# Kernel tuning notes

Measured on AMD Instinct MI355X. Metric: run time of the kernel, lower is better.

## Reference

```python
import jax, jax.numpy as jnp
import numpy as np

B, CM, CT, CA, H, W = 4, 256, 64, 128, 80, 80


def setup_inputs() -> dict:
    key = jax.random.key(0)
    ks = jax.random.split(key, 10)
    s = lambda fan_in: 1.0 / np.sqrt(fan_in)
    return {
        "met_features": jax.random.normal(ks[0], (B, CM, H, W), jnp.float32),
        "terrain_features": jax.random.normal(ks[1], (B, CT, H, W), jnp.float32),
        "wq": jax.random.normal(ks[2], (CA, CM), jnp.float32) * s(CM),
        "bq": jax.random.normal(ks[3], (CA,), jnp.float32) * s(CM),
        "wk": jax.random.normal(ks[4], (CA, CT), jnp.float32) * s(CT),
        "bk": jax.random.normal(ks[5], (CA,), jnp.float32) * s(CT),
        "wv": jax.random.normal(ks[6], (CA, CT), jnp.float32) * s(CT),
        "bv": jax.random.normal(ks[7], (CA,), jnp.float32) * s(CT),
        "wo": jax.random.normal(ks[8], (CM, CA), jnp.float32) * s(CA),
        "bo": jax.random.normal(ks[9], (CM,), jnp.float32) * s(CA),
    }


def reference(met_features, terrain_features, wq, bq, wk, bk, wv, bv, wo, bo):
    b, c, h, w = met_features.shape
    n = h * w  # tokens
    scale = CA ** (-0.5)
    # 1x1 convs == per-pixel linear: [B,Cin,N] -> [B,Cattn,N]
    met = met_features.reshape(b, c, n)
    ter = terrain_features.reshape(b, terrain_features.shape[1], n)
    q = jnp.einsum('oc,bcn->bon', wq, met) + bq[None, :, None]
    k = jnp.einsum('oc,bcn->bon', wk, ter) + bk[None, :, None]
    v = jnp.einsum('oc,bcn->bon', wv, ter) + bv[None, :, None]
    # attn[b, i, j] = sum_c q[b,c,i] * k[b,c,j]
    attn = jax.nn.softmax(jnp.einsum('bci,bcj->bij', q, k) * scale, axis=-1)
    # out[b, c, i] = sum_j v[b,c,j] * attn[b,i,j]
    out = jnp.einsum('bcj,bij->bci', v, attn)
    out = jnp.einsum('oc,bcn->bon', wo, out) + bo[None, :, None]
    return met_features + out.reshape(b, c, h, w)
```

## Files before the change

kernel.cpp:

```cpp
#include <hip/hip_runtime.h>
#include <hip/hip_bf16.h>

#define BB 4
#define CMv 256
#define CTv 64
#define CAv 128
#define NTOK 6400
#define KVSPLIT 5
#define KVRANGE 1280
#define NTILES 20
#define QSCL 0.12753102198064644f

typedef unsigned short u16;
typedef __attribute__((ext_vector_type(8))) short sh8;
typedef __attribute__((ext_vector_type(4))) float f32x4;
typedef __attribute__((ext_vector_type(16))) float f32x16;
typedef __attribute__((ext_vector_type(4))) unsigned uint4v;
typedef __attribute__((ext_vector_type(2))) unsigned uint2v;

__device__ __forceinline__ u16 f2bf(float f) {
  return __builtin_bit_cast(u16, __float2bfloat16(f));
}
__device__ __forceinline__ float bf2f(u16 x) {
  unsigned u = ((unsigned)x) << 16;
  return __builtin_bit_cast(float, u);
}
__device__ __forceinline__ unsigned pk2(float a, float b) {
  unsigned r;
  asm("v_cvt_pk_bf16_f32 %0, %1, %2" : "=v"(r) : "v"(a), "v"(b));
  return r;
}
__device__ __forceinline__ f32x16 zero16() {
  f32x16 z;
#pragma unroll
  for (int i = 0; i < 16; i++) z[i] = 0.f;
  return z;
}
typedef const __attribute__((address_space(1))) unsigned int* gas_p;
typedef __attribute__((address_space(3))) unsigned int* las_p;
__device__ __forceinline__ void gl_lds16(const u16* g, u16* l) {
  __builtin_amdgcn_global_load_lds((gas_p)g, (las_p)l, 16, 0, 0);
}

__global__ __launch_bounds__(256) void prep(const float* __restrict__ wq,
                                            const float* __restrict__ bq,
                                            const float* __restrict__ wk,
                                            const float* __restrict__ wv,
                                            const float* __restrict__ wo,
                                            u16* __restrict__ wqB,
                                            float* __restrict__ bqs,
                                            u16* __restrict__ wkB,
                                            u16* __restrict__ wvB,
                                            u16* __restrict__ woB) {
  const int i0 = blockIdx.x * 256 + threadIdx.x;
  const int stride = gridDim.x * 256;
  for (int i = i0; i < 128 * 256; i += stride) wqB[i] = f2bf(wq[i] * QSCL);
  for (int i = i0; i < 128 * 64; i += stride) { wkB[i] = f2bf(wk[i]); wvB[i] = f2bf(wv[i]); }
  for (int i = i0; i < 256 * 128; i += stride) woB[i] = f2bf(wo[i]);
  for (int i = i0; i < 128; i += stride) bqs[i] = bq[i] * QSCL;
}

__global__ __launch_bounds__(512, 2) void qkvproj(const float* __restrict__ met,
                                                  const float* __restrict__ ter,
                                                  const u16* __restrict__ wqB,
                                                  const float* __restrict__ bqs,
                                                  const u16* __restrict__ wkB,
                                                  const float* __restrict__ bk,
                                                  const u16* __restrict__ wvB,
                                                  const float* __restrict__ bv,
                                                  u16* __restrict__ Qtm,
                                                  u16* __restrict__ Ktm,
                                                  u16* __restrict__ Vcm) {
  const int tid = threadIdx.x;
  const int w = tid >> 6;
  const int lane = tid & 63;
  const int l31 = lane & 31;
  const int h = lane >> 5;

  if (blockIdx.x < 200) {
    const int b = blockIdx.x / 50;
    const int tokb = (blockIdx.x % 50) * 128;
    const int chg = (w & 3) * 32;
    const int half = w >> 2;
    const u16* wb = wqB + (size_t)(chg + l31) * 256 + h * 8;
    sh8 af[16];
#pragma unroll
    for (int kk = 0; kk < 16; kk++) af[kk] = *(const sh8*)(wb + kk * 16);
    float bias[16];
#pragma unroll
    for (int r = 0; r < 16; r++) bias[r] = bqs[chg + (r & 3) + 8 * (r >> 2) + 4 * h];
    const float* mp = met + (size_t)b * CMv * NTOK;
#pragma unroll
    for (int ct = 0; ct < 2; ct++) {
      const int tok = tokb + (half * 2 + ct) * 32 + l31;
      f32x16 acc = zero16();
#pragma unroll
      for (int kk = 0; kk < 16; kk++) {
        const float* cp = mp + (size_t)(kk * 16 + 8 * h) * NTOK + tok;
        float x0 = cp[0], x1 = cp[(size_t)NTOK], x2 = cp[(size_t)2 * NTOK],
              x3 = cp[(size_t)3 * NTOK], x4 = cp[(size_t)4 * NTOK],
              x5 = cp[(size_t)5 * NTOK], x6 = cp[(size_t)6 * NTOK],
              x7 = cp[(size_t)7 * NTOK];
        uint4v u = {pk2(x0, x1), pk2(x2, x3), pk2(x4, x5), pk2(x6, x7)};
        acc = __builtin_amdgcn_mfma_f32_32x32x16_bf16(
            af[kk], __builtin_bit_cast(sh8, u), acc, 0, 0, 0);
      }
      u16* qp = Qtm + ((size_t)b * NTOK + tok) * CAv;
#pragma unroll
      for (int rq = 0; rq < 4; rq++) {
        const int ch0 = chg + 8 * rq + 4 * h;
        uint2v d = {pk2(acc[4 * rq + 0] + bias[4 * rq + 0],
                        acc[4 * rq + 1] + bias[4 * rq + 1]),
                    pk2(acc[4 * rq + 2] + bias[4 * rq + 2],
                        acc[4 * rq + 3] + bias[4 * rq + 3])};
        *(uint2v*)(qp + ch0) = d;
      }
    }
  } else {
    const int bx = blockIdx.x - 200;
    const int b = bx / 50;
    const int tokb = (bx % 50) * 128;
    const bool isV = w >= 4;
    const int chg = (w & 3) * 32;
    const u16* wb = (isV ? wvB : wkB) + (size_t)(chg + l31) * 64 + h * 8;
    sh8 af[4];
#pragma unroll
    for (int kk = 0; kk < 4; kk++) af[kk] = *(const sh8*)(wb + kk * 16);
    const float* barr = isV ? bv : bk;
    float bias[16];
#pragma unroll
    for (int r = 0; r < 16; r++) bias[r] = barr[chg + (r & 3) + 8 * (r >> 2) + 4 * h];
    const float* tp = ter + (size_t)b * CTv * NTOK;
#pragma unroll
    for (int ct = 0; ct < 4; ct++) {
      const int tok = tokb + ct * 32 + l31;
      f32x16 acc = zero16();
#pragma unroll
      for (int kk = 0; kk < 4; kk++) {
        const float* cp = tp + (size_t)(kk * 16 + 8 * h) * NTOK + tok;
        float x0 = cp[0], x1 = cp[(size_t)NTOK], x2 = cp[(size_t)2 * NTOK],
              x3 = cp[(size_t)3 * NTOK], x4 = cp[(size_t)4 * NTOK],
              x5 = cp[(size_t)5 * NTOK], x6 = cp[(size_t)6 * NTOK],
              x7 = cp[(size_t)7 * NTOK];
        uint4v u = {pk2(x0, x1), pk2(x2, x3), pk2(x4, x5), pk2(x6, x7)};
        acc = __builtin_amdgcn_mfma_f32_32x32x16_bf16(
            af[kk], __builtin_bit_cast(sh8, u), acc, 0, 0, 0);
      }
      if (!isV) {
        u16* kp = Ktm + ((size_t)b * NTOK + tok) * CAv;
#pragma unroll
        for (int rq = 0; rq < 4; rq++) {
          const int ch0 = chg + 8 * rq + 4 * h;
          uint2v d = {pk2(acc[4 * rq + 0] + bias[4 * rq + 0],
                          acc[4 * rq + 1] + bias[4 * rq + 1]),
                      pk2(acc[4 * rq + 2] + bias[4 * rq + 2],
                          acc[4 * rq + 3] + bias[4 * rq + 3])};
          *(uint2v*)(kp + ch0) = d;
        }
      } else {
#pragma unroll
        for (int r = 0; r < 16; r++) {
          const int ch = chg + (r & 3) + 8 * (r >> 2) + 4 * h;
          Vcm[((size_t)b * CAv + ch) * NTOK + tok] = f2bf(acc[r] + bias[r]);
        }
      }
    }
  }
}

__global__ __launch_bounds__(512, 2) void attn(const u16* __restrict__ Qtm,
                                               const u16* __restrict__ Ktm,
                                               const u16* __restrict__ Vcm,
                                               u16* __restrict__ Opart,
                                               float* __restrict__ Lpart) {
  __shared__ __align__(16) unsigned char smem[65536];

  const int tid = threadIdx.x;
  const int w = tid >> 6;
  const int lane = tid & 63;
  const int l31 = lane & 31;
  const int h = lane >> 5;

  const int x = blockIdx.x & 7;
  const int W = x * 62 + (x < 4 ? x : 4) + (blockIdx.x >> 3);
  const int g = W / 25;
  const int qt = W % 25;
  const int b = g / KVSPLIT;
  const int kvq = g % KVSPLIT;
  const int qb0 = qt * 256;
  const int kv00 = kvq * KVRANGE;

  const u16* Qb = Qtm + ((size_t)b * NTOK + qb0 + w * 32 + l31) * CAv;
  const u16* Kb = Ktm + (size_t)b * NTOK * CAv;
  const u16* Vb = Vcm + (size_t)b * CAv * NTOK;

  sh8 qf[8];
#pragma unroll
  for (int kk = 0; kk < 8; kk++) qf[kk] = *(const sh8*)(Qb + kk * 16 + h * 8);

  const int kr0 = w * 8 + (lane >> 4);
  const int kr1 = kr0 + 4;
  const u16* ksrc0 = Kb + ((size_t)kv00 + kr0) * CAv + (((lane & 15) ^ (kr0 & 15)) * 8);
  const u16* ksrc1 = Kb + ((size_t)kv00 + kr1) * CAv + (((lane & 15) ^ (kr1 & 15)) * 8);
  const int vc = w * 16 + (lane >> 3);
  const u16* vsrc = Vb + (size_t)vc * NTOK + kv00 +
                    (((lane & 7) ^ ((lane >> 3) & 7)) * 8);

  int koff[8];
#pragma unroll
  for (int kk = 0; kk < 8; kk++)
    koff[kk] = l31 * 256 + (((2 * kk + h) ^ (l31 & 15)) << 4);
  int voff[4];
#pragma unroll
  for (int b2 = 0; b2 < 4; b2++)
    voff[b2] = l31 * 128 + (((2 * b2 + h) ^ (l31 & 7)) << 4);

#define STAGE(p)                                               \
  do {                                                         \
    u16* kb_ = (u16*)(smem + (p) * 32768) + w * 1024;          \
    gl_lds16(ksrc0, kb_);                                      \
    gl_lds16(ksrc1, kb_ + 512);                                \
    u16* vb_ = (u16*)(smem + (p) * 32768 + 16384) + w * 1024;  \
    gl_lds16(vsrc, vb_);                                       \
    gl_lds16(vsrc + (size_t)8 * NTOK, vb_ + 512);              \
    ksrc0 += 64 * CAv;                                         \
    ksrc1 += 64 * CAv;                                         \
    vsrc += 64;                                                \
  } while (0)

  STAGE(0);
  asm volatile("s_waitcnt vmcnt(0)" ::: "memory");
  __builtin_amdgcn_s_barrier();

  f32x16 o[4];
#pragma unroll
  for (int i = 0; i < 4; i++) o[i] = zero16();
  float lsum = 0.f;

  int buf = 0;
  for (int t = 0; t < NTILES; t++) {
    if (t < NTILES - 1) STAGE(buf ^ 1);
    const unsigned char* kbuf = smem + buf * 32768;
    const unsigned char* vbuf = kbuf + 16384;
    __builtin_amdgcn_s_setprio(1);
    f32x16 s0 = zero16(), s1 = zero16();
#pragma unroll
    for (int kk = 0; kk < 8; kk++) {
      sh8 kfa = *(const sh8*)(kbuf + koff[kk]);
      sh8 kfb = *(const sh8*)(kbuf + 8192 + koff[kk]);
      s0 = __builtin_amdgcn_mfma_f32_32x32x16_bf16(kfa, qf[kk], s0, 0, 0, 0);
      s1 = __builtin_amdgcn_mfma_f32_32x32x16_bf16(kfb, qf[kk], s1, 0, 0, 0);
    }
    __builtin_amdgcn_s_setprio(0);
    f32x16 p0, p1;
#pragma unroll
    for (int r = 0; r < 16; r++) {
      p0[r] = __builtin_exp2f(s0[r]);
      p1[r] = __builtin_exp2f(s1[r]);
    }
#pragma unroll
    for (int r = 0; r < 16; r++) lsum += p0[r] + p1[r];
    unsigned pkm0[4][2], pkm1[4][2];
#pragma unroll
    for (int rq = 0; rq < 4; rq++) {
      pkm0[rq][0] = pk2(p0[4 * rq + 0], p0[4 * rq + 1]);
      pkm0[rq][1] = pk2(p0[4 * rq + 2], p0[4 * rq + 3]);
      pkm1[rq][0] = pk2(p1[4 * rq + 0], p1[4 * rq + 1]);
      pkm1[rq][1] = pk2(p1[4 * rq + 2], p1[4 * rq + 3]);
    }
#pragma unroll
    for (int xx = 0; xx < 2; xx++) {
#pragma unroll
      for (int b2i = 0; b2i < 2; b2i++) {
        unsigned ow0, ow1, sd0, sd1;
        if (xx == 0) {
          ow0 = h ? pkm0[2 * b2i + 1][0] : pkm0[2 * b2i][0];
          ow1 = h ? pkm0[2 * b2i + 1][1] : pkm0[2 * b2i][1];
          sd0 = h ? pkm0[2 * b2i][0] : pkm0[2 * b2i + 1][0];
          sd1 = h ? pkm0[2 * b2i][1] : pkm0[2 * b2i + 1][1];
        } else {
          ow0 = h ? pkm1[2 * b2i + 1][0] : pkm1[2 * b2i][0];
          ow1 = h ? pkm1[2 * b2i + 1][1] : pkm1[2 * b2i][1];
          sd0 = h ? pkm1[2 * b2i][0] : pkm1[2 * b2i + 1][0];
          sd1 = h ? pkm1[2 * b2i][1] : pkm1[2 * b2i + 1][1];
        }
        unsigned rv0 = (unsigned)__shfl_xor((int)sd0, 32);
        unsigned rv1 = (unsigned)__shfl_xor((int)sd1, 32);
        uint4v fw = {h ? rv0 : ow0, h ? rv1 : ow1, h ? ow0 : rv0, h ? ow1 : rv1};
        sh8 pf = __builtin_bit_cast(sh8, fw);
        const int b2 = xx * 2 + b2i;
        __builtin_amdgcn_s_setprio(1);
#pragma unroll
        for (int ct = 0; ct < 4; ct++) {
          sh8 vf = *(const sh8*)(vbuf + ct * 4096 + voff[b2]);
          o[ct] = __builtin_amdgcn_mfma_f32_32x32x16_bf16(vf, pf, o[ct], 0, 0, 0);
        }
        __builtin_amdgcn_s_setprio(0);
      }
    }
    asm volatile("s_waitcnt vmcnt(0)" ::: "memory");
    __builtin_amdgcn_s_barrier();
    buf ^= 1;
  }
#undef STAGE

  lsum += __shfl_xor(lsum, 32);
  u16* op = Opart + (((size_t)kvq * BB + b) * NTOK + qb0 + w * 32 + l31) * CAv;
#pragma unroll
  for (int ct = 0; ct < 4; ct++)
#pragma unroll
    for (int rq = 0; rq < 4; rq++) {
      uint2v d = {pk2(o[ct][4 * rq + 0], o[ct][4 * rq + 1]),
                  pk2(o[ct][4 * rq + 2], o[ct][4 * rq + 3])};
      *(uint2v*)(op + ct * 32 + rq * 8 + h * 4) = d;
    }
  if (h == 0) {
    size_t mi = ((size_t)kvq * BB + b) * NTOK + qb0 + w * 32 + l31;
    Lpart[mi] = lsum;
  }
}

__global__ __launch_bounds__(512, 2) void outproj(const float* __restrict__ met,
                                                  const u16* __restrict__ woB,
                                                  const float* __restrict__ bo,
                                                  const u16* __restrict__ Opart,
                                                  const float* __restrict__ Lpart,
                                                  float* __restrict__ out) {
  const int tid = threadIdx.x;
  const int w = tid >> 6;
  const int lane = tid & 63;
  const int l31 = lane & 31;
  const int h = lane >> 5;

  const int b = blockIdx.x / 100;
  const int tokb = (blockIdx.x % 100) * 64;
  const int chg = (w & 3) * 64;
  const int ct = w >> 2;
  const int tok = tokb + ct * 32 + l31;
  const size_t n = (size_t)b * NTOK + tok;
  const size_t PSTR = (size_t)BB * NTOK;

  const u16* wb0 = woB + (size_t)(chg + l31) * 128 + h * 8;
  const u16* wb1 = woB + (size_t)(chg + 32 + l31) * 128 + h * 8;
  sh8 a0[8], a1[8];
#pragma unroll
  for (int kk = 0; kk < 8; kk++) {
    a0[kk] = *(const sh8*)(wb0 + kk * 16);
    a1[kk] = *(const sh8*)(wb1 + kk * 16);
  }

  float L = 0.f;
#pragma unroll
  for (int i = 0; i < KVSPLIT; i++) L += Lpart[i * PSTR + n];
  const float rL = 1.f / L;

  f32x16 acc0 = zero16(), acc1 = zero16();
#pragma unroll
  for (int kk = 0; kk < 8; kk++) {
    float s[8];
#pragma unroll
    for (int j = 0; j < 8; j++) s[j] = 0.f;
#pragma unroll
    for (int i = 0; i < KVSPLIT; i++) {
      sh8 v = *(const sh8*)(Opart + (i * PSTR + n) * CAv + kk * 16 + 8 * h);
#pragma unroll
      for (int j = 0; j < 8; j++) s[j] += bf2f((u16)v[j]);
    }
    uint4v u = {pk2(s[0] * rL, s[1] * rL), pk2(s[2] * rL, s[3] * rL),
                pk2(s[4] * rL, s[5] * rL), pk2(s[6] * rL, s[7] * rL)};
    sh8 bf = __builtin_bit_cast(sh8, u);
    acc0 = __builtin_amdgcn_mfma_f32_32x32x16_bf16(a0[kk], bf, acc0, 0, 0, 0);
    acc1 = __builtin_amdgcn_mfma_f32_32x32x16_bf16(a1[kk], bf, acc1, 0, 0, 0);
  }
#pragma unroll
  for (int r = 0; r < 16; r++) {
    const int ro = (r & 3) + 8 * (r >> 2) + 4 * h;
    const int ch0 = chg + ro;
    const int ch1 = chg + 32 + ro;
    size_t i0 = ((size_t)b * CMv + ch0) * NTOK + tok;
    size_t i1 = ((size_t)b * CMv + ch1) * NTOK + tok;
    out[i0] = met[i0] + acc0[r] + bo[ch0];
    out[i1] = met[i1] + acc1[r] + bo[ch1];
  }
}

extern "C" void kernel_launch(void* const* d_in, const int* in_sizes, int n_in,
                              void* d_out, int out_size, void* d_ws, size_t ws_size,
                              hipStream_t stream) {
  const float* met = (const float*)d_in[0];
  const float* ter = (const float*)d_in[1];
  const float* wq = (const float*)d_in[2];
  const float* bq = (const float*)d_in[3];
  const float* wk = (const float*)d_in[4];
  const float* bk = (const float*)d_in[5];
  const float* wv = (const float*)d_in[6];
  const float* bv = (const float*)d_in[7];
  const float* wo = (const float*)d_in[8];
  const float* bo = (const float*)d_in[9];
  float* out = (float*)d_out;

  u16* Qtm = (u16*)d_ws;
  u16* Ktm = Qtm + (size_t)BB * NTOK * CAv;
  u16* Vcm = Ktm + (size_t)BB * NTOK * CAv;
  u16* Opart = Vcm + (size_t)BB * NTOK * CAv;
  float* Lpart = (float*)(Opart + (size_t)KVSPLIT * BB * NTOK * CAv);
  u16* wqB = (u16*)(Lpart + (size_t)KVSPLIT * BB * NTOK);
  u16* wkB = wqB + 128 * 256;
  u16* wvB = wkB + 128 * 64;
  u16* woB = wvB + 128 * 64;
  float* bqs = (float*)(woB + 256 * 128);

  prep<<<dim3(40), dim3(256), 0, stream>>>(wq, bq, wk, wv, wo, wqB, bqs, wkB, wvB, woB);
  qkvproj<<<dim3(400), dim3(512), 0, stream>>>(met, ter, wqB, bqs, wkB, bk,
                                               wvB, bv, Qtm, Ktm, Vcm);
  attn<<<dim3(500), dim3(512), 0, stream>>>(Qtm, Ktm, Vcm, Opart, Lpart);
  outproj<<<dim3(400), dim3(512), 0, stream>>>(met, woB, bo, Opart, Lpart, out);
}
```

Baseline: 171.4 us.

## Triple-buffer smaller 32-key KV tiles to raise attention kernel occupancy

Halves the KV tile size from 64 to 32 keys per iteration, so each tile buffer uses 16KB. It switches from double to triple buffering with two tiles in flight, and partial vmcnt waits let loads overlap more. Total LDS drops to 48KB and launch bounds rise to 4 blocks per SM. In exchange there are twice as many barriers per KV range, less MFMA work between syncs, and more register pressure from the tighter launch bound.

```diff
diff --git a/kernel.cpp b/kernel.cpp
--- a/kernel.cpp
+++ b/kernel.cpp
@@ -8,7 +8,7 @@
 #define NTOK 6400
 #define KVSPLIT 5
 #define KVRANGE 1280
-#define NTILES 20
+#define NTILES 40
 #define QSCL 0.12753102198064644f
 
 typedef unsigned short u16;
@@ -168,12 +168,12 @@
   }
 }
 
-__global__ __launch_bounds__(512, 2) void attn(const u16* __restrict__ Qtm,
+__global__ __launch_bounds__(512, 4) void attn(const u16* __restrict__ Qtm,
                                                const u16* __restrict__ Ktm,
                                                const u16* __restrict__ Vcm,
                                                u16* __restrict__ Opart,
                                                float* __restrict__ Lpart) {
-  __shared__ __align__(16) unsigned char smem[65536];
+  __shared__ __align__(16) unsigned char smem[49152];
 
   const int tid = threadIdx.x;
   const int w = tid >> 6;
@@ -198,38 +198,34 @@
 #pragma unroll
   for (int kk = 0; kk < 8; kk++) qf[kk] = *(const sh8*)(Qb + kk * 16 + h * 8);
 
-  const int kr0 = w * 8 + (lane >> 4);
-  const int kr1 = kr0 + 4;
-  const u16* ksrc0 = Kb + ((size_t)kv00 + kr0) * CAv + (((lane & 15) ^ (kr0 & 15)) * 8);
-  const u16* ksrc1 = Kb + ((size_t)kv00 + kr1) * CAv + (((lane & 15) ^ (kr1 & 15)) * 8);
-  const int vc = w * 16 + (lane >> 3);
+  const int kr = w * 4 + (lane >> 4);
+  const u16* ksrc = Kb + ((size_t)kv00 + kr) * CAv + (((lane & 15) ^ (kr & 15)) * 8);
+  const int vc = w * 16 + (lane >> 2);
   const u16* vsrc = Vb + (size_t)vc * NTOK + kv00 +
-                    (((lane & 7) ^ ((lane >> 3) & 7)) * 8);
+                    (((lane & 3) ^ ((lane >> 3) & 3)) * 8);
 
   int koff[8];
 #pragma unroll
   for (int kk = 0; kk < 8; kk++)
     koff[kk] = l31 * 256 + (((2 * kk + h) ^ (l31 & 15)) << 4);
-  int voff[4];
-#pragma unroll
-  for (int b2 = 0; b2 < 4; b2++)
-    voff[b2] = l31 * 128 + (((2 * b2 + h) ^ (l31 & 7)) << 4);
-
-#define STAGE(p)                                               \
-  do {                                                         \
-    u16* kb_ = (u16*)(smem + (p) * 32768) + w * 1024;          \
-    gl_lds16(ksrc0, kb_);                                      \
-    gl_lds16(ksrc1, kb_ + 512);                                \
-    u16* vb_ = (u16*)(smem + (p) * 32768 + 16384) + w * 1024;  \
-    gl_lds16(vsrc, vb_);                                       \
-    gl_lds16(vsrc + (size_t)8 * NTOK, vb_ + 512);              \
-    ksrc0 += 64 * CAv;                                         \
-    ksrc1 += 64 * CAv;                                         \
-    vsrc += 64;                                                \
+  int voff[2];
+#pragma unroll
+  for (int b2 = 0; b2 < 2; b2++)
+    voff[b2] = l31 * 64 + (((2 * b2 + h) ^ ((l31 >> 1) & 3)) << 4);
+
+#define STAGE(p)                                              \
+  do {                                                        \
+    u16* kb_ = (u16*)(smem + (p) * 16384) + w * 512;          \
+    gl_lds16(ksrc, kb_);                                      \
+    u16* vb_ = (u16*)(smem + (p) * 16384 + 8192) + w * 512;   \
+    gl_lds16(vsrc, vb_);                                      \
+    ksrc += 32 * CAv;                                         \
+    vsrc += 32;                                               \
   } while (0)
 
   STAGE(0);
-  asm volatile("s_waitcnt vmcnt(0)" ::: "memory");
+  STAGE(1);
+  asm volatile("s_waitcnt vmcnt(2)" ::: "memory");
   __builtin_amdgcn_s_barrier();
 
   f32x16 o[4];
@@ -237,70 +233,61 @@
   for (int i = 0; i < 4; i++) o[i] = zero16();
   float lsum = 0.f;
 
-  int buf = 0;
+  int buf = 0, sb = 2;
   for (int t = 0; t < NTILES; t++) {
-    if (t < NTILES - 1) STAGE(buf ^ 1);
-    const unsigned char* kbuf = smem + buf * 32768;
-    const unsigned char* vbuf = kbuf + 16384;
+    if (t < NTILES - 2) STAGE(sb);
+    const unsigned char* kbuf = smem + buf * 16384;
+    const unsigned char* vbuf = kbuf + 8192;
     __builtin_amdgcn_s_setprio(1);
-    f32x16 s0 = zero16(), s1 = zero16();
+    f32x16 s = zero16();
 #pragma unroll
     for (int kk = 0; kk < 8; kk++) {
-      sh8 kfa = *(const sh8*)(kbuf + koff[kk]);
-      sh8 kfb = *(const sh8*)(kbuf + 8192 + koff[kk]);
-      s0 = __builtin_amdgcn_mfma_f32_32x32x16_bf16(kfa, qf[kk], s0, 0, 0, 0);
-      s1 = __builtin_amdgcn_mfma_f32_32x32x16_bf16(kfb, qf[kk], s1, 0, 0, 0);
+      sh8 kf = *(const sh8*)(kbuf + koff[kk]);
+      s = __builtin_amdgcn_mfma_f32_32x32x16_bf16(kf, qf[kk], s, 0, 0, 0);
     }
     __builtin_amdgcn_s_setprio(0);
-    f32x16 p0, p1;
-#pragma unroll
-    for (int r = 0; r < 16; r++) {
-      p0[r] = __builtin_exp2f(s0[r]);
-      p1[r] = __builtin_exp2f(s1[r]);
-    }
-#pragma unroll
-    for (int r = 0; r < 16; r++) lsum += p0[r] + p1[r];
-    unsigned pkm0[4][2], pkm1[4][2];
+    f32x16 p;
+#pragma unroll
+    for (int r = 0; r < 16; r++) p[r] = __builtin_exp2f(s[r]);
+    {
+      float t0 = (p[0] + p[1]) + (p[2] + p[3]);
+      float t1 = (p[4] + p[5]) + (p[6] + p[7]);
+      float t2 = (p[8] + p[9]) + (p[10] + p[11]);
+      float t3 = (p[12] + p[13]) + (p[14] + p[15]);
+      lsum += (t0 + t1) + (t2 + t3);
+    }
+    unsigned pkm[4][2];
 #pragma unroll
     for (int rq = 0; rq < 4; rq++) {
-      pkm0[rq][0] = pk2(p0[4 * rq + 0], p0[4 * rq + 1]);
-      pkm0[rq][1] = pk2(p0[4 * rq + 2], p0[4 * rq + 3]);
-      pkm1[rq][0] = pk2(p1[4 * rq + 0], p1[4 * rq + 1]);
-      pkm1[rq][1] = pk2(p1[4 * rq + 2], p1[4 * rq + 3]);
-    }
-#pragma unroll
-    for (int xx = 0; xx < 2; xx++) {
-#pragma unroll
-      for (int b2i = 0; b2i < 2; b2i++) {
-        unsigned ow0, ow1, sd0, sd1;
-        if (xx == 0) {
-          ow0 = h ? pkm0[2 * b2i + 1][0] : pkm0[2 * b2i][0];
-          ow1 = h ? pkm0[2 * b2i + 1][1] : pkm0[2 * b2i][1];
-          sd0 = h ? pkm0[2 * b2i][0] : pkm0[2 * b2i + 1][0];
-          sd1 = h ? pkm0[2 * b2i][1] : pkm0[2 * b2i + 1][1];
-        } else {
-          ow0 = h ? pkm1[2 * b2i + 1][0] : pkm1[2 * b2i][0];
-          ow1 = h ? pkm1[2 * b2i + 1][1] : pkm1[2 * b2i][1];
-          sd0 = h ? pkm1[2 * b2i][0] : pkm1[2 * b2i + 1][0];
-          sd1 = h ? pkm1[2 * b2i][1] : pkm1[2 * b2i + 1][1];
-        }
-        unsigned rv0 = (unsigned)__shfl_xor((int)sd0, 32);
-        unsigned rv1 = (unsigned)__shfl_xor((int)sd1, 32);
-        uint4v fw = {h ? rv0 : ow0, h ? rv1 : ow1, h ? ow0 : rv0, h ? ow1 : rv1};
-        sh8 pf = __builtin_bit_cast(sh8, fw);
-        const int b2 = xx * 2 + b2i;
-        __builtin_amdgcn_s_setprio(1);
-#pragma unroll
-        for (int ct = 0; ct < 4; ct++) {
-          sh8 vf = *(const sh8*)(vbuf + ct * 4096 + voff[b2]);
-          o[ct] = __builtin_amdgcn_mfma_f32_32x32x16_bf16(vf, pf, o[ct], 0, 0, 0);
-        }
-        __builtin_amdgcn_s_setprio(0);
+      pkm[rq][0] = pk2(p[4 * rq + 0], p[4 * rq + 1]);
+      pkm[rq][1] = pk2(p[4 * rq + 2], p[4 * rq + 3]);
+    }
+#pragma unroll
+    for (int b2 = 0; b2 < 2; b2++) {
+      unsigned ow0 = h ? pkm[2 * b2 + 1][0] : pkm[2 * b2][0];
+      unsigned ow1 = h ? pkm[2 * b2 + 1][1] : pkm[2 * b2][1];
+      unsigned sd0 = h ? pkm[2 * b2][0] : pkm[2 * b2 + 1][0];
+      unsigned sd1 = h ? pkm[2 * b2][1] : pkm[2 * b2 + 1][1];
+      unsigned rv0 = (unsigned)__shfl_xor((int)sd0, 32);
+      unsigned rv1 = (unsigned)__shfl_xor((int)sd1, 32);
+      uint4v fw = {h ? rv0 : ow0, h ? rv1 : ow1, h ? ow0 : rv0, h ? ow1 : rv1};
+      sh8 pf = __builtin_bit_cast(sh8, fw);
+      __builtin_amdgcn_s_setprio(1);
+#pragma unroll
+      for (int ct = 0; ct < 4; ct++) {
+        sh8 vf = *(const sh8*)(vbuf + ct * 2048 + voff[b2]);
+        o[ct] = __builtin_amdgcn_mfma_f32_32x32x16_bf16(vf, pf, o[ct], 0, 0, 0);
       }
-    }
-    asm volatile("s_waitcnt vmcnt(0)" ::: "memory");
+      __builtin_amdgcn_s_setprio(0);
+    }
+    if (t < NTILES - 2) {
+      asm volatile("s_waitcnt vmcnt(2)" ::: "memory");
+    } else {
+      asm volatile("s_waitcnt vmcnt(0)" ::: "memory");
+    }
     __builtin_amdgcn_s_barrier();
-    buf ^= 1;
+    buf = (buf == 2) ? 0 : buf + 1;
+    sb = (sb == 2) ? 0 : sb + 1;
   }
 #undef STAGE
 
```

Measured after the change: 210.9 us. 23.1% more time.

## Split attention PV channels across wave pairs and double the grid

Applied to the files above, without the earlier changes.

Each block now covers 128 queries instead of 256. Pairs of waves share the same 32 query rows, and each wave computes the PV product for half of the value channels. This halves the output accumulators per wave and raises the launch-bounds occupancy hint, doubling the grid to 1000 blocks. In exchange, the QK^T MFMAs and exponentials are computed redundantly in both waves of a pair, and K/V tiles are staged from global memory twice as often overall.

```diff
diff --git a/kernel.cpp b/kernel.cpp
--- a/kernel.cpp
+++ b/kernel.cpp
@@ -168,7 +168,7 @@
   }
 }
 
-__global__ __launch_bounds__(512, 2) void attn(const u16* __restrict__ Qtm,
+__global__ __launch_bounds__(512, 4) void attn(const u16* __restrict__ Qtm,
                                                const u16* __restrict__ Ktm,
                                                const u16* __restrict__ Vcm,
                                                u16* __restrict__ Opart,
@@ -180,17 +180,19 @@
   const int lane = tid & 63;
   const int l31 = lane & 31;
   const int h = lane >> 5;
+  const int q = w & 3;
+  const int dh = w >> 2;
 
   const int x = blockIdx.x & 7;
-  const int W = x * 62 + (x < 4 ? x : 4) + (blockIdx.x >> 3);
-  const int g = W / 25;
-  const int qt = W % 25;
+  const int W = x * 125 + (blockIdx.x >> 3);
+  const int g = W / 50;
+  const int qt = W % 50;
   const int b = g / KVSPLIT;
   const int kvq = g % KVSPLIT;
-  const int qb0 = qt * 256;
+  const int qb0 = qt * 128;
   const int kv00 = kvq * KVRANGE;
 
-  const u16* Qb = Qtm + ((size_t)b * NTOK + qb0 + w * 32 + l31) * CAv;
+  const u16* Qb = Qtm + ((size_t)b * NTOK + qb0 + q * 32 + l31) * CAv;
   const u16* Kb = Ktm + (size_t)b * NTOK * CAv;
   const u16* Vb = Vcm + (size_t)b * CAv * NTOK;
 
@@ -232,9 +234,9 @@
   asm volatile("s_waitcnt vmcnt(0)" ::: "memory");
   __builtin_amdgcn_s_barrier();
 
-  f32x16 o[4];
-#pragma unroll
-  for (int i = 0; i < 4; i++) o[i] = zero16();
+  f32x16 o[2];
+  o[0] = zero16();
+  o[1] = zero16();
   float lsum = 0.f;
 
   int buf = 0;
@@ -242,31 +244,46 @@
     if (t < NTILES - 1) STAGE(buf ^ 1);
     const unsigned char* kbuf = smem + buf * 32768;
     const unsigned char* vbuf = kbuf + 16384;
-    __builtin_amdgcn_s_setprio(1);
-    f32x16 s0 = zero16(), s1 = zero16();
-#pragma unroll
-    for (int kk = 0; kk < 8; kk++) {
-      sh8 kfa = *(const sh8*)(kbuf + koff[kk]);
-      sh8 kfb = *(const sh8*)(kbuf + 8192 + koff[kk]);
-      s0 = __builtin_amdgcn_mfma_f32_32x32x16_bf16(kfa, qf[kk], s0, 0, 0, 0);
-      s1 = __builtin_amdgcn_mfma_f32_32x32x16_bf16(kfb, qf[kk], s1, 0, 0, 0);
-    }
-    __builtin_amdgcn_s_setprio(0);
-    f32x16 p0, p1;
-#pragma unroll
-    for (int r = 0; r < 16; r++) {
-      p0[r] = __builtin_exp2f(s0[r]);
-      p1[r] = __builtin_exp2f(s1[r]);
-    }
-#pragma unroll
-    for (int r = 0; r < 16; r++) lsum += p0[r] + p1[r];
     unsigned pkm0[4][2], pkm1[4][2];
-#pragma unroll
-    for (int rq = 0; rq < 4; rq++) {
-      pkm0[rq][0] = pk2(p0[4 * rq + 0], p0[4 * rq + 1]);
-      pkm0[rq][1] = pk2(p0[4 * rq + 2], p0[4 * rq + 3]);
-      pkm1[rq][0] = pk2(p1[4 * rq + 0], p1[4 * rq + 1]);
-      pkm1[rq][1] = pk2(p1[4 * rq + 2], p1[4 * rq + 3]);
+    {
+      __builtin_amdgcn_s_setprio(1);
+      f32x16 s = zero16();
+#pragma unroll
+      for (int kk = 0; kk < 8; kk++) {
+        sh8 kf = *(const sh8*)(kbuf + koff[kk]);
+        s = __builtin_amdgcn_mfma_f32_32x32x16_bf16(kf, qf[kk], s, 0, 0, 0);
+      }
+      __builtin_amdgcn_s_setprio(0);
+#pragma unroll
+      for (int rq = 0; rq < 4; rq++) {
+        float e0 = __builtin_exp2f(s[4 * rq + 0]);
+        float e1 = __builtin_exp2f(s[4 * rq + 1]);
+        float e2 = __builtin_exp2f(s[4 * rq + 2]);
+        float e3 = __builtin_exp2f(s[4 * rq + 3]);
+        lsum += (e0 + e1) + (e2 + e3);
+        pkm0[rq][0] = pk2(e0, e1);
+        pkm0[rq][1] = pk2(e2, e3);
+      }
+    }
+    {
+      __builtin_amdgcn_s_setprio(1);
+      f32x16 s = zero16();
+#pragma unroll
+      for (int kk = 0; kk < 8; kk++) {
+        sh8 kf = *(const sh8*)(kbuf + 8192 + koff[kk]);
+        s = __builtin_amdgcn_mfma_f32_32x32x16_bf16(kf, qf[kk], s, 0, 0, 0);
+      }
+      __builtin_amdgcn_s_setprio(0);
+#pragma unroll
+      for (int rq = 0; rq < 4; rq++) {
+        float e0 = __builtin_exp2f(s[4 * rq + 0]);
+        float e1 = __builtin_exp2f(s[4 * rq + 1]);
+        float e2 = __builtin_exp2f(s[4 * rq + 2]);
+        float e3 = __builtin_exp2f(s[4 * rq + 3]);
+        lsum += (e0 + e1) + (e2 + e3);
+        pkm1[rq][0] = pk2(e0, e1);
+        pkm1[rq][1] = pk2(e2, e3);
+      }
     }
 #pragma unroll
     for (int xx = 0; xx < 2; xx++) {
@@ -291,8 +308,8 @@
         const int b2 = xx * 2 + b2i;
         __builtin_amdgcn_s_setprio(1);
 #pragma unroll
-        for (int ct = 0; ct < 4; ct++) {
-          sh8 vf = *(const sh8*)(vbuf + ct * 4096 + voff[b2]);
+        for (int ct = 0; ct < 2; ct++) {
+          sh8 vf = *(const sh8*)(vbuf + (dh * 2 + ct) * 4096 + voff[b2]);
           o[ct] = __builtin_amdgcn_mfma_f32_32x32x16_bf16(vf, pf, o[ct], 0, 0, 0);
         }
         __builtin_amdgcn_s_setprio(0);
@@ -305,17 +322,17 @@
 #undef STAGE
 
   lsum += __shfl_xor(lsum, 32);
-  u16* op = Opart + (((size_t)kvq * BB + b) * NTOK + qb0 + w * 32 + l31) * CAv;
-#pragma unroll
-  for (int ct = 0; ct < 4; ct++)
+  u16* op = Opart + (((size_t)kvq * BB + b) * NTOK + qb0 + q * 32 + l31) * CAv + dh * 64;
+#pragma unroll
+  for (int ct = 0; ct < 2; ct++)
 #pragma unroll
     for (int rq = 0; rq < 4; rq++) {
       uint2v d = {pk2(o[ct][4 * rq + 0], o[ct][4 * rq + 1]),
                   pk2(o[ct][4 * rq + 2], o[ct][4 * rq + 3])};
       *(uint2v*)(op + ct * 32 + rq * 8 + h * 4) = d;
     }
-  if (h == 0) {
-    size_t mi = ((size_t)kvq * BB + b) * NTOK + qb0 + w * 32 + l31;
+  if (h == 0 && dh == 0) {
+    size_t mi = ((size_t)kvq * BB + b) * NTOK + qb0 + q * 32 + l31;
     Lpart[mi] = lsum;
   }
 }
@@ -413,6 +430,6 @@
   prep<<<dim3(40), dim3(256), 0, stream>>>(wq, bq, wk, wv, wo, wqB, bqs, wkB, wvB, woB);
   qkvproj<<<dim3(400), dim3(512), 0, stream>>>(met, ter, wqB, bqs, wkB, bk,
                                                wvB, bv, Qtm, Ktm, Vcm);
-  attn<<<dim3(500), dim3(512), 0, stream>>>(Qtm, Ktm, Vcm, Opart, Lpart);
+  attn<<<dim3(1000), dim3(512), 0, stream>>>(Qtm, Ktm, Vcm, Opart, Lpart);
   outproj<<<dim3(400), dim3(512), 0, stream>>>(met, woB, bo, Opart, Lpart, out);
 }
```

Result: slower. 234.4 us (+36.8%).
